# Kernel optimization log

Hardware: AMD Instinct MI355X
Metric: run time of the kernel (lower is better)

The kernel has to match this reference:

```python
import jax, jax.numpy as jnp
from jax import lax
import numpy as np

P, K1, K2 = 8, 5, 9  # nPaths, small/large ECA kernel sizes (from nDim=1024, nPaths=8)
LN_EPS = 1e-5


def setup_inputs() -> dict:
    key = jax.random.key(0)
    ks = jax.random.split(key, 6)
    b, c, l = 16, 1024, 4096
    return {
        "x": jax.random.normal(ks[0], (b, c, l), dtype=jnp.float32),
        "conv1_w": jax.random.normal(ks[1], (P, K1), dtype=jnp.float32) * 0.3,
        "conv2_w": jax.random.normal(ks[2], (P, K2), dtype=jnp.float32) * 0.3,
        "combine_w": jax.random.normal(ks[3], (2,), dtype=jnp.float32) * 0.5,
        "combine_b": jnp.zeros((), dtype=jnp.float32),
        "ln_g": jnp.ones((P,), dtype=jnp.float32),
        "ln_b": jnp.zeros((P,), dtype=jnp.float32),
        "W1": jax.random.normal(ks[4], (P, 2 * P), dtype=jnp.float32) * 0.3,
        "b1": jnp.zeros((2 * P,), dtype=jnp.float32),
        "W2": jax.random.normal(ks[5], (2 * P, P), dtype=jnp.float32) * 0.3,
        "b2": jnp.zeros((P,), dtype=jnp.float32),
    }


def _grouped_conv(y, w):
    # y: (b, P, D) pooled per-path features; w: (P, k) one 1-ch kernel per path.
    # Equivalent to the per-path Conv1d(1,1,k, padding=(k-1)//2) loop, fused.
    k = w.shape[-1]
    pad = (k - 1) // 2
    return lax.conv_general_dilated(
        y, w[:, None, :], window_strides=(1,), padding=[(pad, pad)],
        dimension_numbers=("NCH", "OIH", "NCH"), feature_group_count=y.shape[1])


def reference(x, conv1_w, conv2_w, combine_w, combine_b, ln_g, ln_b, W1, b1, W2, b2):
    b, c, l = x.shape
    nP = conv1_w.shape[0]
    D = c // nP
    pf = x.reshape(b, nP, D, l)          # (b, P, D, l)
    y = pf.mean(-1)                      # (b, P, D) global-avg-pool over l
    y1 = _grouped_conv(y, conv1_w)       # (b, P, D)
    y2 = _grouped_conv(y, conv2_w)       # (b, P, D)
    # combine = Conv1d(2,1,1): scalar mix of the two conv outputs + bias
    attn = jax.nn.sigmoid(combine_w[0] * y1 + combine_w[1] * y2 + combine_b)
    # cross-path gating MLP on per-path mean attention
    cross = attn.mean(-1)                # (b, P)
    mu = cross.mean(-1, keepdims=True)
    var = cross.var(-1, keepdims=True)   # biased, matches torch LayerNorm
    h = (cross - mu) / jnp.sqrt(var + LN_EPS) * ln_g + ln_b
    h = jax.nn.gelu(h @ W1 + b1, approximate=False)
    gate = jax.nn.sigmoid(h @ W2 + b2)   # (b, P)
    scale = attn * gate[:, :, None]      # (b, P, D)
    out = pf * scale[..., None]          # broadcast over l
    return out.reshape(b, c, l)
```

## Files before the change

### kernel.cpp

```cpp
#include <hip/hip_runtime.h>
#include <math.h>

#define NP 8
#define ND 128
#define NC 1024
#define NL 4096
#define NB 16
#define LN_EPS 1e-5f

typedef float v4f __attribute__((ext_vector_type(4)));

__global__ __launch_bounds__(256) void pool_kernel(const float* __restrict__ x,
                                                   float* __restrict__ y) {
    const int wid  = threadIdx.x >> 6;
    const int lane = threadIdx.x & 63;
    const int row  = blockIdx.x * 4 + wid;
    const v4f* xr = (const v4f*)(x + (size_t)row * NL);
    float s = 0.f;
    #pragma unroll
    for (int i = 0; i < 16; ++i) {
        v4f v = xr[lane + i * 64];
        s += v.x + v.y + v.z + v.w;
    }
    #pragma unroll
    for (int off = 32; off; off >>= 1) s += __shfl_down(s, off, 64);
    if (lane == 0) y[row] = s * (1.f / NL);
}

__global__ __launch_bounds__(1024) void attn_kernel(
    const float* __restrict__ y,
    const float* __restrict__ conv1_w,
    const float* __restrict__ conv2_w,
    const float* __restrict__ combine_w,
    const float* __restrict__ combine_b,
    const float* __restrict__ ln_g, const float* __restrict__ ln_b,
    const float* __restrict__ W1, const float* __restrict__ b1,
    const float* __restrict__ W2, const float* __restrict__ b2,
    float* __restrict__ scale)
{
    const int b = blockIdx.x;
    const int tid = threadIdx.x;
    const int p = tid >> 7;
    const int d = tid & 127;

    __shared__ float sy[NC];
    __shared__ float sattn[NC];
    __shared__ float sred[16];
    __shared__ float sgate[NP];

    sy[tid] = y[b * NC + tid];
    __syncthreads();

    const float* rowp = sy + p * ND;
    float c1 = 0.f;
    #pragma unroll
    for (int t = 0; t < 5; ++t) {
        int dd = d + t - 2;
        float v = (dd >= 0 && dd < ND) ? rowp[dd] : 0.f;
        c1 += conv1_w[p * 5 + t] * v;
    }
    float c2 = 0.f;
    #pragma unroll
    for (int t = 0; t < 9; ++t) {
        int dd = d + t - 4;
        float v = (dd >= 0 && dd < ND) ? rowp[dd] : 0.f;
        c2 += conv2_w[p * 9 + t] * v;
    }
    const float z = combine_w[0] * c1 + combine_w[1] * c2 + combine_b[0];
    const float a = 1.f / (1.f + expf(-z));
    sattn[tid] = a;

    float r = a;
    #pragma unroll
    for (int off = 32; off; off >>= 1) r += __shfl_down(r, off, 64);
    const int lane = tid & 63, wid = tid >> 6;
    if (lane == 0) sred[wid] = r;
    __syncthreads();

    if (tid == 0) {
        float cross[NP];
        #pragma unroll
        for (int pp = 0; pp < NP; ++pp)
            cross[pp] = (sred[2 * pp] + sred[2 * pp + 1]) * (1.f / ND);
        float mu = 0.f;
        #pragma unroll
        for (int pp = 0; pp < NP; ++pp) mu += cross[pp];
        mu *= (1.f / NP);
        float var = 0.f;
        #pragma unroll
        for (int pp = 0; pp < NP; ++pp) { float dl = cross[pp] - mu; var += dl * dl; }
        var *= (1.f / NP);
        const float inv = rsqrtf(var + LN_EPS);
        float h[NP];
        #pragma unroll
        for (int pp = 0; pp < NP; ++pp)
            h[pp] = (cross[pp] - mu) * inv * ln_g[pp] + ln_b[pp];
        float h2[2 * NP];
        for (int j = 0; j < 2 * NP; ++j) {
            float s = b1[j];
            #pragma unroll
            for (int pp = 0; pp < NP; ++pp) s += h[pp] * W1[pp * (2 * NP) + j];
            h2[j] = 0.5f * s * (1.f + erff(s * 0.70710678118654752f));
        }
        for (int pp = 0; pp < NP; ++pp) {
            float s = b2[pp];
            #pragma unroll
            for (int j = 0; j < 2 * NP; ++j) s += h2[j] * W2[j * NP + pp];
            sgate[pp] = 1.f / (1.f + expf(-s));
        }
    }
    __syncthreads();

    scale[b * NC + tid] = sattn[tid] * sgate[p];
}

__global__ __launch_bounds__(256) void scale_kernel(const float* __restrict__ x,
                                                    const float* __restrict__ scale,
                                                    float* __restrict__ out) {
    const v4f* xv = (const v4f*)x;
    v4f* ov = (v4f*)out;
    const size_t n = (size_t)NB * NC * (NL / 4);
    const size_t stride = (size_t)gridDim.x * blockDim.x;
    for (size_t i = (size_t)blockIdx.x * blockDim.x + threadIdx.x; i < n; i += stride) {
        const float s = scale[i >> 10];
        v4f v = xv[i];
        v *= s;
        __builtin_nontemporal_store(v, &ov[i]);
    }
}

extern "C" void kernel_launch(void* const* d_in, const int* in_sizes, int n_in,
                              void* d_out, int out_size, void* d_ws, size_t ws_size,
                              hipStream_t stream) {
    const float* x         = (const float*)d_in[0];
    const float* conv1_w   = (const float*)d_in[1];
    const float* conv2_w   = (const float*)d_in[2];
    const float* combine_w = (const float*)d_in[3];
    const float* combine_b = (const float*)d_in[4];
    const float* ln_g      = (const float*)d_in[5];
    const float* ln_b      = (const float*)d_in[6];
    const float* W1        = (const float*)d_in[7];
    const float* b1        = (const float*)d_in[8];
    const float* W2        = (const float*)d_in[9];
    const float* b2        = (const float*)d_in[10];
    float* out = (float*)d_out;

    float* y     = (float*)d_ws;
    float* scale = y + NB * NC;

    pool_kernel<<<NB * NC / 4, 256, 0, stream>>>(x, y);
    attn_kernel<<<NB, 1024, 0, stream>>>(y, conv1_w, conv2_w, combine_w, combine_b,
                                         ln_g, ln_b, W1, b1, W2, b2, scale);
    scale_kernel<<<2048, 256, 0, stream>>>(x, scale, out);
}
```

Baseline: 133.0 us.

## Fuse pool, attention and scaling into one cooperative kernel with register-held x

Replaces the three-kernel pool/attn/scale pipeline with a single cooperative kernel. Each block loads 8 rows of x into registers, reduces them to pooled means, and waits at a grid-wide sync. It then redundantly computes the per-batch conv/gate math in shared memory and scales the register-resident x, so the second global read of x is dropped. The design depends on 2048 blocks being co-resident, which means 8 blocks per CU. Holding 128 floats of x per thread at that occupancy risks heavy register spills, and the kernel also adds grid-sync and redundant per-block attention cost. It falls back to the old path when occupancy is insufficient.

```diff
diff --git a/kernel.cpp b/kernel.cpp
--- a/kernel.cpp
+++ b/kernel.cpp
@@ -1,5 +1,8 @@
 #include <hip/hip_runtime.h>
+#include <hip/hip_cooperative_groups.h>
 #include <math.h>
+
+namespace cg = cooperative_groups;
 
 #define NP 8
 #define ND 128
@@ -8,7 +11,143 @@
 #define NB 16
 #define LN_EPS 1e-5f
 
+#define NBLK 2048
+#define RPB 8
+
 typedef float v4f __attribute__((ext_vector_type(4)));
+
+__device__ __forceinline__ void attn_math(const float* __restrict__ sy,
+                                          float* __restrict__ sattn,
+                                          const float* conv1_w, const float* conv2_w,
+                                          const float* combine_w, const float* combine_b,
+                                          int tid) {
+    #pragma unroll
+    for (int k = 0; k < 4; ++k) {
+        const int pos = tid + 256 * k;
+        const int p = pos >> 7, d = pos & 127;
+        const float* rowp = sy + p * ND;
+        float c1 = 0.f;
+        #pragma unroll
+        for (int t = 0; t < 5; ++t) {
+            int dd = d + t - 2;
+            float v = (dd >= 0 && dd < ND) ? rowp[dd] : 0.f;
+            c1 += conv1_w[p * 5 + t] * v;
+        }
+        float c2 = 0.f;
+        #pragma unroll
+        for (int t = 0; t < 9; ++t) {
+            int dd = d + t - 4;
+            float v = (dd >= 0 && dd < ND) ? rowp[dd] : 0.f;
+            c2 += conv2_w[p * 9 + t] * v;
+        }
+        const float z = combine_w[0] * c1 + combine_w[1] * c2 + combine_b[0];
+        sattn[pos] = 1.f / (1.f + expf(-z));
+    }
+}
+
+__device__ __forceinline__ void gate_math(const float* __restrict__ scross,
+                                          float* __restrict__ sgate,
+                                          const float* ln_g, const float* ln_b,
+                                          const float* W1, const float* b1,
+                                          const float* W2, const float* b2) {
+    float cross[NP];
+    #pragma unroll
+    for (int pp = 0; pp < NP; ++pp) cross[pp] = scross[pp];
+    float mu = 0.f;
+    #pragma unroll
+    for (int pp = 0; pp < NP; ++pp) mu += cross[pp];
+    mu *= (1.f / NP);
+    float var = 0.f;
+    #pragma unroll
+    for (int pp = 0; pp < NP; ++pp) { float dl = cross[pp] - mu; var += dl * dl; }
+    var *= (1.f / NP);
+    const float inv = rsqrtf(var + LN_EPS);
+    float h[NP];
+    #pragma unroll
+    for (int pp = 0; pp < NP; ++pp)
+        h[pp] = (cross[pp] - mu) * inv * ln_g[pp] + ln_b[pp];
+    float h2[2 * NP];
+    for (int j = 0; j < 2 * NP; ++j) {
+        float s = b1[j];
+        #pragma unroll
+        for (int pp = 0; pp < NP; ++pp) s += h[pp] * W1[pp * (2 * NP) + j];
+        h2[j] = 0.5f * s * (1.f + erff(s * 0.70710678118654752f));
+    }
+    for (int pp = 0; pp < NP; ++pp) {
+        float s = b2[pp];
+        #pragma unroll
+        for (int j = 0; j < 2 * NP; ++j) s += h2[j] * W2[j * NP + pp];
+        sgate[pp] = 1.f / (1.f + expf(-s));
+    }
+}
+
+__global__ __launch_bounds__(256, 8) void fused_kernel(
+    const float* __restrict__ x, float* __restrict__ y,
+    const float* __restrict__ conv1_w, const float* __restrict__ conv2_w,
+    const float* __restrict__ combine_w, const float* __restrict__ combine_b,
+    const float* __restrict__ ln_g, const float* __restrict__ ln_b,
+    const float* __restrict__ W1, const float* __restrict__ b1,
+    const float* __restrict__ W2, const float* __restrict__ b2,
+    float* __restrict__ out)
+{
+    const int tid  = threadIdx.x;
+    const int row0 = blockIdx.x * RPB;
+    const int b    = row0 >> 10;
+    const int p0   = (row0 & (NC - 1)) >> 7;
+
+    __shared__ float sred[RPB][4];
+    __shared__ float sy[NC];
+    __shared__ float sattn[NC];
+    __shared__ float scross[NP];
+    __shared__ float sgate[NP];
+
+    v4f xd[RPB][4];
+    const v4f* xb = (const v4f*)x + (size_t)row0 * (NL / 4);
+    v4f* ob       = (v4f*)out    + (size_t)row0 * (NL / 4);
+
+    #pragma unroll
+    for (int r = 0; r < RPB; ++r) {
+        float ps = 0.f;
+        #pragma unroll
+        for (int k = 0; k < 4; ++k) {
+            xd[r][k] = xb[(size_t)r * (NL / 4) + tid + 256 * k];
+            ps += xd[r][k].x + xd[r][k].y + xd[r][k].z + xd[r][k].w;
+        }
+        #pragma unroll
+        for (int off = 32; off; off >>= 1) ps += __shfl_down(ps, off, 64);
+        if ((tid & 63) == 0) sred[r][tid >> 6] = ps;
+    }
+    __syncthreads();
+    if (tid < RPB)
+        y[row0 + tid] = (sred[tid][0] + sred[tid][1] + sred[tid][2] + sred[tid][3]) * (1.f / NL);
+    __threadfence();
+    cg::this_grid().sync();
+
+    #pragma unroll
+    for (int k = 0; k < 4; ++k) sy[tid + 256 * k] = y[b * NC + tid + 256 * k];
+    __syncthreads();
+    attn_math(sy, sattn, conv1_w, conv2_w, combine_w, combine_b, tid);
+    __syncthreads();
+    if (tid < NP) {
+        float s = 0.f;
+        for (int d = 0; d < ND; ++d) s += sattn[tid * ND + d];
+        scross[tid] = s * (1.f / ND);
+    }
+    __syncthreads();
+    if (tid == 0) gate_math(scross, sgate, ln_g, ln_b, W1, b1, W2, b2);
+    __syncthreads();
+
+    const float g = sgate[p0];
+    #pragma unroll
+    for (int r = 0; r < RPB; ++r) {
+        const float s = sattn[(row0 & (NC - 1)) + r] * g;
+        #pragma unroll
+        for (int k = 0; k < 4; ++k) {
+            v4f v = xd[r][k] * s;
+            __builtin_nontemporal_store(v, &ob[(size_t)r * (NL / 4) + tid + 256 * k]);
+        }
+    }
+}
 
 __global__ __launch_bounds__(256) void pool_kernel(const float* __restrict__ x,
                                                    float* __restrict__ y) {
@@ -29,10 +168,8 @@
 
 __global__ __launch_bounds__(1024) void attn_kernel(
     const float* __restrict__ y,
-    const float* __restrict__ conv1_w,
-    const float* __restrict__ conv2_w,
-    const float* __restrict__ combine_w,
-    const float* __restrict__ combine_b,
+    const float* __restrict__ conv1_w, const float* __restrict__ conv2_w,
+    const float* __restrict__ combine_w, const float* __restrict__ combine_b,
     const float* __restrict__ ln_g, const float* __restrict__ ln_b,
     const float* __restrict__ W1, const float* __restrict__ b1,
     const float* __restrict__ W2, const float* __restrict__ b2,
@@ -78,36 +215,11 @@
     __syncthreads();
 
     if (tid == 0) {
-        float cross[NP];
+        float scross[NP];
         #pragma unroll
         for (int pp = 0; pp < NP; ++pp)
-            cross[pp] = (sred[2 * pp] + sred[2 * pp + 1]) * (1.f / ND);
-        float mu = 0.f;
-        #pragma unroll
-        for (int pp = 0; pp < NP; ++pp) mu += cross[pp];
-        mu *= (1.f / NP);
-        float var = 0.f;
-        #pragma unroll
-        for (int pp = 0; pp < NP; ++pp) { float dl = cross[pp] - mu; var += dl * dl; }
-        var *= (1.f / NP);
-        const float inv = rsqrtf(var + LN_EPS);
-        float h[NP];
-        #pragma unroll
-        for (int pp = 0; pp < NP; ++pp)
-            h[pp] = (cross[pp] - mu) * inv * ln_g[pp] + ln_b[pp];
-        float h2[2 * NP];
-        for (int j = 0; j < 2 * NP; ++j) {
-            float s = b1[j];
-            #pragma unroll
-            for (int pp = 0; pp < NP; ++pp) s += h[pp] * W1[pp * (2 * NP) + j];
-            h2[j] = 0.5f * s * (1.f + erff(s * 0.70710678118654752f));
-        }
-        for (int pp = 0; pp < NP; ++pp) {
-            float s = b2[pp];
-            #pragma unroll
-            for (int j = 0; j < 2 * NP; ++j) s += h2[j] * W2[j * NP + pp];
-            sgate[pp] = 1.f / (1.f + expf(-s));
-        }
+            scross[pp] = (sred[2 * pp] + sred[2 * pp + 1]) * (1.f / ND);
+        gate_math(scross, sgate, ln_g, ln_b, W1, b1, W2, b2);
     }
     __syncthreads();
 
@@ -148,8 +260,21 @@
     float* y     = (float*)d_ws;
     float* scale = y + NB * NC;
 
-    pool_kernel<<<NB * NC / 4, 256, 0, stream>>>(x, y);
-    attn_kernel<<<NB, 1024, 0, stream>>>(y, conv1_w, conv2_w, combine_w, combine_b,
-                                         ln_g, ln_b, W1, b1, W2, b2, scale);
-    scale_kernel<<<2048, 256, 0, stream>>>(x, scale, out);
-}
+    int nb = 0;
+    hipOccupancyMaxActiveBlocksPerMultiprocessor(&nb, fused_kernel, 256, 0);
+    if (nb >= NBLK / 256) {
+        void* args[] = { (void*)&x, (void*)&y,
+                         (void*)&conv1_w, (void*)&conv2_w,
+                         (void*)&combine_w, (void*)&combine_b,
+                         (void*)&ln_g, (void*)&ln_b,
+                         (void*)&W1, (void*)&b1, (void*)&W2, (void*)&b2,
+                         (void*)&out };
+        hipLaunchCooperativeKernel((const void*)fused_kernel, dim3(NBLK), dim3(256),
+                                   args, 0, stream);
+    } else {
+        pool_kernel<<<NB * NC / 4, 256, 0, stream>>>(x, y);
+        attn_kernel<<<NB, 1024, 0, stream>>>(y, conv1_w, conv2_w, combine_w, combine_b,
+                                             ln_g, ln_b, W1, b1, W2, b2, scale);
+        scale_kernel<<<2048, 256, 0, stream>>>(x, scale, out);
+    }
+}
```

New measurement: 133.3 us. About the same (+0.2%).
